# Optimization experiments

Hardware: AMD Instinct MI355X
Metric: run time of the kernel (lower is better)

The kernel has to match this reference:

```python
import jax, jax.numpy as jnp
import numpy as np

B, C_IN, H, W = 2, 256, 48, 48
OC, G, KH, KW, PH, PW = 256, 4, 7, 7, 3, 3


def _patches(y, Hn, Wn):
    # y: (B, C, Hp, Wp) -> (B, C, KH, KW, Hn, Wn); stride=1, dilation=1
    return jnp.stack([
        jnp.stack([y[:, :, i:i + Hn, j:j + Wn] for j in range(KW)], axis=2)
        for i in range(KH)
    ], axis=2)


def setup_inputs() -> dict:
    key = jax.random.key(0)
    k1, k2, k3, k4 = jax.random.split(key, 4)
    fan_out = 3 * OC  # 1x1 conv, kaiming fan_out
    conv_w = jax.random.normal(k2, (3 * OC, C_IN), dtype=jnp.float32) * np.sqrt(2.0 / fan_out).astype(np.float32)
    return {
        "x": jax.random.normal(k1, (B, C_IN, H, W), dtype=jnp.float32),
        "conv_w": conv_w,
        "rpe_h": jax.random.normal(k3, (G, 1, KH, 1, (OC // G) // 2), dtype=jnp.float32),
        "rpe_w": jax.random.normal(k4, (G, 1, 1, KW, (OC // G) // 2), dtype=jnp.float32),
    }


def reference(x, conv_w, rpe_h, rpe_w):
    b, c, h, w = x.shape
    goc = OC // G
    c2 = goc // 2
    K = KH * KW
    center = (K - 1) // 2
    ci, cj = center // KW, center % KW

    # 1x1 conv to 3*OC channels, then zero-pad (equiv. to Conv2d(padding) + bias=False)
    y = jnp.einsum('bchw,oc->bohw', x, conv_w)
    y = jnp.pad(y, ((0, 0), (0, 0), (PH, PH), (PW, PW)))
    Hn = h + 2 * PH - (KH - 1)
    Wn = w + 2 * PW - (KW - 1)
    P = Hn * Wn

    q_full, k_full, v_full = jnp.split(y, 3, axis=1)

    # query: only the center element of each window is used
    query = q_full[:, :, ci:ci + Hn, cj:cj + Wn].reshape(b, G, goc, P)
    query = jnp.transpose(query, (0, 1, 3, 2))  # (B,G,P,goc)

    # key: full windows + relative position embeddings
    kp = _patches(k_full, Hn, Wn).reshape(b, G, goc, KH, KW, P)
    key = jnp.transpose(kp, (0, 1, 5, 3, 4, 2))  # (B,G,P,KH,KW,goc)
    key = jnp.concatenate((key[..., :c2] + rpe_h, key[..., c2:] + rpe_w), axis=1)  # (B,2G,P,KH,KW,c2)
    key = key.reshape(b, G, P, K, goc)  # row-major reshape matches torch

    vp = _patches(v_full, Hn, Wn).reshape(b, G, goc, K, P)
    value = jnp.transpose(vp, (0, 1, 4, 3, 2))  # (B,G,P,K,goc)

    att = jax.nn.softmax(jnp.einsum('bgpc,bgpkc->bgpk', query, key), axis=-1)
    out = jnp.einsum('bgpk,bgpkc->bgpc', att, value)  # (B,G,P,goc)
    out = jnp.transpose(out, (0, 1, 3, 2)).reshape(b, OC, Hn, Wn)
    return out
```

## Files before the change

kernel.cpp:

```cpp
#include <hip/hip_runtime.h>

#define BB   2
#define CIN  256
#define OC3  768
#define NG   4
#define GOC  64
#define C2   32
#define KK   49
#define PP   2304
#define HALF_P 1152

#define RS      56
#define BROWS   54
#define BSTRIDE (BROWS * RS * OC3)
#define IOFF    ((3 * RS + 3) * OC3)

#define Y2_BYTES  (BB * BROWS * RS * OC3 * 4)
#define XT_OFF    Y2_BYTES
#define WT_OFF    (XT_OFF + BB * PP * 512 * 2)

typedef __attribute__((ext_vector_type(8))) short bf16x8;
typedef __attribute__((ext_vector_type(4))) float f32x4;

static __device__ __forceinline__ unsigned short f2bf_rne(float x) {
    unsigned int u = __float_as_uint(x);
    unsigned int r = u + 0x7FFFu + ((u >> 16) & 1u);
    return (unsigned short)(r >> 16);
}
static __device__ __forceinline__ float bf2f(unsigned short h) {
    return __uint_as_float(((unsigned int)h) << 16);
}

#define ROW4  (RS * OC3 / 4)
#define REG1  (6 * ROW4)
#define COLS4 (OC3 / 4)
__global__ __launch_bounds__(256) void zero_guard(float* __restrict__ Y2)
{
    const int idx = blockIdx.x * 256 + threadIdx.x;
    const int b   = blockIdx.y;
    float4* Yb = (float4*)(Y2 + (size_t)b * BSTRIDE);
    const float4 z = make_float4(0.f, 0.f, 0.f, 0.f);
    if (idx < REG1) {
        int r6  = idx / ROW4;
        int rem = idx - r6 * ROW4;
        int r   = (r6 < 3) ? r6 : 48 + r6;
        Yb[r * ROW4 + rem] = z;
    } else {
        int i2  = idx - REG1;
        int r   = 3 + i2 / (8 * COLS4);
        int rem = i2 - (r - 3) * (8 * COLS4);
        int cg  = rem / COLS4;
        int c   = (cg < 3) ? cg : 48 + cg;
        int ch4 = rem - cg * COLS4;
        Yb[(r * RS + c) * COLS4 + ch4] = z;
    }
}

__global__ __launch_bounds__(256) void convert_w(
    const float* __restrict__ W, short* __restrict__ Wt)
{
    int t = blockIdx.x * 256 + threadIdx.x;
    int o = t >> 8, c = t & 255;
    float v = W[t];
    unsigned short hi = f2bf_rne(v);
    unsigned short lo = f2bf_rne(v - bf2f(hi));
    Wt[(size_t)o * 512 + c]       = (short)hi;
    Wt[(size_t)o * 512 + 256 + c] = (short)lo;
}

__global__ __launch_bounds__(256) void convert_x(
    const float* __restrict__ X, short* __restrict__ Xt)
{
    __shared__ float tile[64][65];
    const int t  = threadIdx.x;
    const int p0 = blockIdx.x * 64;
    const int c0 = blockIdx.y * 64;
    const int b  = blockIdx.z;

    const float* Xb = X + (size_t)b * CIN * PP;
    #pragma unroll
    for (int r = 0; r < 16; ++r) {
        int idx = r * 256 + t;
        int c = idx >> 6, p = idx & 63;
        tile[c][p] = Xb[(size_t)(c0 + c) * PP + p0 + p];
    }
    __syncthreads();
    short* Xo = Xt + (size_t)b * PP * 512;
    #pragma unroll
    for (int r = 0; r < 16; ++r) {
        int idx = r * 256 + t;
        int p = idx >> 6, c = idx & 63;
        float v = tile[c][p];
        unsigned short hi = f2bf_rne(v);
        unsigned short lo = f2bf_rne(v - bf2f(hi));
        size_t base = (size_t)(p0 + p) * 512 + c0 + c;
        Xo[base]       = (short)hi;
        Xo[base + 256] = (short)lo;
    }
}

#define LDA 40

__global__ __launch_bounds__(256, 4) void conv_mfma(
    const short* __restrict__ Wt,
    const short* __restrict__ Xt,
    float* __restrict__ Y2)
{
    __shared__ short As[64 * LDA];
    __shared__ short Bs[64 * LDA];

    const int tid = threadIdx.x;
    const int bn  = blockIdx.x;
    const int bm  = blockIdx.y;
    const int b   = blockIdx.z;
    const int om0 = bm * 64, pn0 = bn * 64;

    const int lane = tid & 63, w = tid >> 6;
    const int oq = (w & 1) * 32, pq = (w >> 1) * 32;
    const int ln15 = lane & 15, q = lane >> 4;

    const int  lrow  = (tid & 127) >> 1;
    const int  lsoff = (tid & 1) * 16;
    const bool isA   = tid < 128;
    const short* gA = Wt + (size_t)(om0 + lrow) * 512 + lsoff;
    const short* gB = Xt + (size_t)b * PP * 512 + (size_t)(pn0 + lrow) * 512 + lsoff;
    const short* gsrc = isA ? gA : gB;
    short* ldst = (isA ? As : Bs) + lrow * LDA + lsoff;

    f32x4 acc[2][2] = {};

    for (int k0 = 0; k0 < 768; k0 += 32) {
        const int wk = (k0 < 256) ? k0 : k0 - 256;
        const int xk = (k0 < 512) ? k0 : k0 - 512;
        const int kk = isA ? wk : xk;
        uint4 v0 = *(const uint4*)(gsrc + kk);
        uint4 v1 = *(const uint4*)(gsrc + kk + 8);
        __syncthreads();
        *(uint4*)ldst       = v0;
        *(uint4*)(ldst + 8) = v1;
        __syncthreads();

        bf16x8 af[2], bf[2];
        #pragma unroll
        for (int i = 0; i < 2; ++i) {
            af[i] = *(const bf16x8*)&As[(oq + i * 16 + ln15) * LDA + q * 8];
            bf[i] = *(const bf16x8*)&Bs[(pq + i * 16 + ln15) * LDA + q * 8];
        }
        #pragma unroll
        for (int i = 0; i < 2; ++i)
            #pragma unroll
            for (int j = 0; j < 2; ++j)
                acc[i][j] = __builtin_amdgcn_mfma_f32_16x16x32_bf16(
                    af[i], bf[j], acc[i][j], 0, 0, 0);
    }

    float* Yb = Y2 + (size_t)b * BSTRIDE + IOFF;
    #pragma unroll
    for (int i = 0; i < 2; ++i) {
        #pragma unroll
        for (int j = 0; j < 2; ++j) {
            int o = om0 + oq + i * 16 + q * 4;
            int p = pn0 + pq + j * 16 + ln15;
            int h = p / 48, ww = p - h * 48;
            *(f32x4*)&Yb[(size_t)(h * RS + ww) * OC3 + o] = acc[i][j];
        }
    }
}

struct TagH { static constexpr bool value = true;  };
struct TagW { static constexpr bool value = false; };

__global__ __launch_bounds__(256, 4) void attn_kernel(
    const float* __restrict__ Y2,
    const float* __restrict__ rpe_h,
    const float* __restrict__ rpe_w,
    float* __restrict__ out)
{
    __shared__ float xpose[4][65];

    const int tid  = threadIdx.x;
    const int lane = tid & 63;
    const int w    = tid >> 6;
    const int bx     = blockIdx.x;
    const int wblock = (bx & 7) * 576 + (bx >> 3);
    const int wid    = wblock * 4 + w;
    const int pq   = wid % PP;
    const int g    = (wid / PP) & (NG - 1);
    const int b    = wid / (PP * NG);
    const int ph   = pq / 48;
    const int pw   = pq - ph * 48;

    const float* Yb = Y2 + (size_t)b * BSTRIDE + IOFF;

    const float qv = Yb[(size_t)(ph * RS + pw) * OC3 + g * GOC + lane];

    const int t   = (pq >= HALF_P) ? 1 : 0;
    const int qpr = pq - t * HALF_P;
    const int p0  = 2 * qpr;
    const int ph0 = p0 / 48;
    const int pw0 = p0 - ph0 * 48;
    const int g2  = 2 * g + t;
    const bool use_h = (g2 < NG);
    const int  kch   = use_h ? (CIN + g2 * GOC) : (CIN + (g2 - NG) * GOC + C2);
    const float* rb  = use_h ? (rpe_h + g2 * 7 * C2) : (rpe_w + (g2 - NG) * 7 * C2);

    const int  c  = lane & 31;
    const bool hi = (lane >= 32);

    const float R0 = rb[0 * C2 + c], R1 = rb[1 * C2 + c], R2 = rb[2 * C2 + c],
                R3 = rb[3 * C2 + c], R4 = rb[4 * C2 + c], R5 = rb[5 * C2 + c],
                R6 = rb[6 * C2 + c];

    const float* kb = Yb + (size_t)(ph0 * RS + pw0) * OC3 + kch + c;

    auto rget = [&](int idx) -> float {
        return idx == 0 ? R0 : idx == 1 ? R1 : idx == 2 ? R2 :
               idx == 3 ? R3 : idx == 4 ? R4 : idx == 5 ? R5 : R6;
    };

    auto tree = [&](auto tag) -> float {
        constexpr bool UH = decltype(tag)::value;
        auto chunkprod = [&](int l) -> float {
            int m0 = 2 * l,     h10 = (m0 >= KK), k0 = m0 - KK * h10;
            int m1 = 2 * l + 1, h11 = (m1 >= KK), k1 = m1 - KK * h11;
            int i0 = k0 / 7, j0 = k0 % 7, i1 = k1 / 7, j1 = k1 % 7;
            int d0 = ((i0 - 3) * RS + (h10 + j0 - 3)) * OC3;
            int d1 = ((i1 - 3) * RS + (h11 + j1 - 3)) * OC3;
            float kv = kb[hi ? d1 : d0];
            float ra = UH ? rget(i0) : rget(j0);
            float rc = UH ? rget(i1) : rget(j1);
            kv += hi ? rc : ra;
            return qv * kv;
        };
        float sv[32];
        #pragma unroll
        for (int jj = 0; jj < 32; ++jj) {
            if (2 * jj >= KK) { sv[jj] = 0.f; continue; }
            float pa = chunkprod(2 * jj);
            float pb = (2 * jj + 1 < KK) ? chunkprod(2 * jj + 1) : 0.f;
            float u  = (lane & 1) ? pb : pa;
            float ww = (lane & 1) ? pa : pb;
            sv[jj] = u + __shfl_xor(ww, 1, 64);
        }
        #pragma unroll
        for (int d = 2; d < 64; d <<= 1) {
            #pragma unroll
            for (int i = 0; i < 32; i += d) {
                float a  = sv[i], bb = sv[i + d / 2];
                float u  = (lane & d) ? bb : a;
                float ww = (lane & d) ? a : bb;
                sv[i] = u + __shfl_xor(ww, d, 64);
            }
        }
        return sv[0];
    };

    const float logit = use_h ? tree(TagH{}) : tree(TagW{});

    float mx = logit;
    #pragma unroll
    for (int d = 1; d < 64; d <<= 1)
        mx = fmaxf(mx, __shfl_xor(mx, d, 64));
    float e = (lane < KK) ? __expf(logit - mx) : 0.f;
    float ssum = e;
    #pragma unroll
    for (int d = 1; d < 64; d <<= 1)
        ssum += __shfl_xor(ssum, d, 64);
    const float att = e / ssum;

    float acc = 0.f;
    const float* vb = Yb + (size_t)(ph * RS + pw) * OC3 + 2 * CIN + g * GOC + lane;
    #pragma unroll
    for (int k = 0; k < KK; ++k) {
        int i = k / 7, j = k % 7;
        int doff = ((i - 3) * RS + (j - 3)) * OC3;
        float ak = __uint_as_float(
            __builtin_amdgcn_readlane(__float_as_uint(att), k));
        acc = fmaf(ak, vb[doff], acc);
    }

    xpose[w][lane] = acc;
    __syncthreads();
    const int wid0 = wblock * 4;
    const int pq0  = wid0 % PP;
    const int g0   = (wid0 / PP) & (NG - 1);
    const int b0   = wid0 / (PP * NG);
    const int ch   = tid >> 2;
    const int w2   = tid & 3;
    out[((size_t)b0 * 256 + g0 * GOC + ch) * PP + pq0 + w2] = xpose[w2][ch];
}

extern "C" void kernel_launch(void* const* d_in, const int* in_sizes, int n_in,
                              void* d_out, int out_size, void* d_ws, size_t ws_size,
                              hipStream_t stream)
{
    const float* x  = (const float*)d_in[0];
    const float* w  = (const float*)d_in[1];
    const float* rh = (const float*)d_in[2];
    const float* rw = (const float*)d_in[3];

    float* Y2 = (float*)d_ws;
    short* Xt = (short*)((char*)d_ws + XT_OFF);
    short* Wt = (short*)((char*)d_ws + WT_OFF);

    zero_guard<<<dim3(540, BB), 256, 0, stream>>>(Y2);
    convert_w<<<768, 256, 0, stream>>>(w, Wt);
    convert_x<<<dim3(36, 4, BB), 256, 0, stream>>>(x, Xt);

    conv_mfma<<<dim3(36, 12, BB), 256, 0, stream>>>(Wt, Xt, Y2);

    attn_kernel<<<(BB * NG * PP) / 4, 256, 0, stream>>>(Y2, rh, rw, (float*)d_out);
}
```

Before: 117.4 us.

## Stage attention key/value/query windows in shared memory and merge prep kernels

The attention kernel now cooperatively loads the 7x14 key window, the 7x10 value window and the four queries for its block of adjacent pixels into LDS with float4 loads. Each wave then reads its neighbourhood from shared memory instead of doing strided scalar global loads, so overlapping windows are not fetched again. Separately, the zero-guard, weight-conversion and input-conversion kernels are merged into one launch to cut launch overhead. The cost is more LDS per block, which may lower occupancy, plus an extra block-wide barrier.

New measurement: 123.2 us. 5.0% more time.

```diff
diff --git a/kernel.cpp b/kernel.cpp
--- a/kernel.cpp
+++ b/kernel.cpp
@@ -22,6 +22,9 @@
 typedef __attribute__((ext_vector_type(8))) short bf16x8;
 typedef __attribute__((ext_vector_type(4))) float f32x4;
 
+struct TagH { static constexpr bool value = true;  };
+struct TagW { static constexpr bool value = false; };
+
 static __device__ __forceinline__ unsigned short f2bf_rne(float x) {
     unsigned int u = __float_as_uint(x);
     unsigned int r = u + 0x7FFFu + ((u >> 16) & 1u);
@@ -34,68 +37,65 @@
 #define ROW4  (RS * OC3 / 4)
 #define REG1  (6 * ROW4)
 #define COLS4 (OC3 / 4)
-__global__ __launch_bounds__(256) void zero_guard(float* __restrict__ Y2)
+__global__ __launch_bounds__(256) void prep(
+    const float* __restrict__ X, const float* __restrict__ W,
+    float* __restrict__ Y2, short* __restrict__ Xt, short* __restrict__ Wt)
 {
-    const int idx = blockIdx.x * 256 + threadIdx.x;
-    const int b   = blockIdx.y;
-    float4* Yb = (float4*)(Y2 + (size_t)b * BSTRIDE);
-    const float4 z = make_float4(0.f, 0.f, 0.f, 0.f);
-    if (idx < REG1) {
-        int r6  = idx / ROW4;
-        int rem = idx - r6 * ROW4;
-        int r   = (r6 < 3) ? r6 : 48 + r6;
-        Yb[r * ROW4 + rem] = z;
-    } else {
-        int i2  = idx - REG1;
-        int r   = 3 + i2 / (8 * COLS4);
-        int rem = i2 - (r - 3) * (8 * COLS4);
-        int cg  = rem / COLS4;
-        int c   = (cg < 3) ? cg : 48 + cg;
-        int ch4 = rem - cg * COLS4;
-        Yb[(r * RS + c) * COLS4 + ch4] = z;
-    }
-}
-
-__global__ __launch_bounds__(256) void convert_w(
-    const float* __restrict__ W, short* __restrict__ Wt)
-{
-    int t = blockIdx.x * 256 + threadIdx.x;
-    int o = t >> 8, c = t & 255;
-    float v = W[t];
-    unsigned short hi = f2bf_rne(v);
-    unsigned short lo = f2bf_rne(v - bf2f(hi));
-    Wt[(size_t)o * 512 + c]       = (short)hi;
-    Wt[(size_t)o * 512 + 256 + c] = (short)lo;
-}
-
-__global__ __launch_bounds__(256) void convert_x(
-    const float* __restrict__ X, short* __restrict__ Xt)
-{
-    __shared__ float tile[64][65];
-    const int t  = threadIdx.x;
-    const int p0 = blockIdx.x * 64;
-    const int c0 = blockIdx.y * 64;
-    const int b  = blockIdx.z;
-
-    const float* Xb = X + (size_t)b * CIN * PP;
-    #pragma unroll
-    for (int r = 0; r < 16; ++r) {
-        int idx = r * 256 + t;
-        int c = idx >> 6, p = idx & 63;
-        tile[c][p] = Xb[(size_t)(c0 + c) * PP + p0 + p];
-    }
-    __syncthreads();
-    short* Xo = Xt + (size_t)b * PP * 512;
-    #pragma unroll
-    for (int r = 0; r < 16; ++r) {
-        int idx = r * 256 + t;
-        int p = idx >> 6, c = idx & 63;
-        float v = tile[c][p];
+    const int bxx = blockIdx.x;
+    const int tid = threadIdx.x;
+    if (bxx < 1080) {
+        const int b   = bxx / 540;
+        const int idx = (bxx - b * 540) * 256 + tid;
+        float4* Yb = (float4*)(Y2 + (size_t)b * BSTRIDE);
+        const float4 z = make_float4(0.f, 0.f, 0.f, 0.f);
+        if (idx < REG1) {
+            int r6  = idx / ROW4;
+            int rem = idx - r6 * ROW4;
+            int r   = (r6 < 3) ? r6 : 48 + r6;
+            Yb[r * ROW4 + rem] = z;
+        } else {
+            int i2  = idx - REG1;
+            int r   = 3 + i2 / (8 * COLS4);
+            int rem = i2 - (r - 3) * (8 * COLS4);
+            int cg  = rem / COLS4;
+            int c   = (cg < 3) ? cg : 48 + cg;
+            int ch4 = rem - cg * COLS4;
+            Yb[(r * RS + c) * COLS4 + ch4] = z;
+        }
+    } else if (bxx < 1848) {
+        int t = (bxx - 1080) * 256 + tid;
+        int o = t >> 8, c = t & 255;
+        float v = W[t];
         unsigned short hi = f2bf_rne(v);
         unsigned short lo = f2bf_rne(v - bf2f(hi));
-        size_t base = (size_t)(p0 + p) * 512 + c0 + c;
-        Xo[base]       = (short)hi;
-        Xo[base + 256] = (short)lo;
+        Wt[(size_t)o * 512 + c]       = (short)hi;
+        Wt[(size_t)o * 512 + 256 + c] = (short)lo;
+    } else {
+        __shared__ float tile[64][65];
+        const int cx = bxx - 1848;
+        const int p0 = (cx % 36) * 64;
+        const int c0 = ((cx / 36) & 3) * 64;
+        const int b  = cx / 144;
+        const float* Xb = X + (size_t)b * CIN * PP;
+        #pragma unroll
+        for (int r = 0; r < 16; ++r) {
+            int idx = r * 256 + tid;
+            int c = idx >> 6, p = idx & 63;
+            tile[c][p] = Xb[(size_t)(c0 + c) * PP + p0 + p];
+        }
+        __syncthreads();
+        short* Xo = Xt + (size_t)b * PP * 512;
+        #pragma unroll
+        for (int r = 0; r < 16; ++r) {
+            int idx = r * 256 + tid;
+            int p = idx >> 6, c = idx & 63;
+            float v = tile[c][p];
+            unsigned short hi = f2bf_rne(v);
+            unsigned short lo = f2bf_rne(v - bf2f(hi));
+            size_t base = (size_t)(p0 + p) * 512 + c0 + c;
+            Xo[base]       = (short)hi;
+            Xo[base + 256] = (short)lo;
+        }
     }
 }
 
@@ -167,15 +167,15 @@
     }
 }
 
-struct TagH { static constexpr bool value = true;  };
-struct TagW { static constexpr bool value = false; };
-
 __global__ __launch_bounds__(256, 4) void attn_kernel(
     const float* __restrict__ Y2,
     const float* __restrict__ rpe_h,
     const float* __restrict__ rpe_w,
     float* __restrict__ out)
 {
+    __shared__ float Ks[7 * 14 * 32];
+    __shared__ float Vs[7 * 10 * 64];
+    __shared__ float Qs[4 * 64];
     __shared__ float xpose[4][65];
 
     const int tid  = threadIdx.x;
@@ -183,35 +183,60 @@
     const int w    = tid >> 6;
     const int bx     = blockIdx.x;
     const int wblock = (bx & 7) * 576 + (bx >> 3);
-    const int wid    = wblock * 4 + w;
-    const int pq   = wid % PP;
-    const int g    = (wid / PP) & (NG - 1);
-    const int b    = wid / (PP * NG);
-    const int ph   = pq / 48;
-    const int pw   = pq - ph * 48;
-
-    const float* Yb = Y2 + (size_t)b * BSTRIDE + IOFF;
-
-    const float qv = Yb[(size_t)(ph * RS + pw) * OC3 + g * GOC + lane];
-
-    const int t   = (pq >= HALF_P) ? 1 : 0;
-    const int qpr = pq - t * HALF_P;
-    const int p0  = 2 * qpr;
-    const int ph0 = p0 / 48;
-    const int pw0 = p0 - ph0 * 48;
-    const int g2  = 2 * g + t;
+    const int wid0   = wblock * 4;
+    const int pq0  = wid0 % PP;
+    const int g    = (wid0 / PP) & (NG - 1);
+    const int b    = wid0 / (PP * NG);
+    const int ph   = pq0 / 48;
+    const int pws  = pq0 - ph * 48;
+    const int t    = (pq0 >= HALF_P) ? 1 : 0;
+    const int qp0  = pq0 - t * HALF_P;
+    const int p00  = 2 * qp0;
+    const int ph0  = p00 / 48;
+    const int w0   = p00 - ph0 * 48;
+    const int g2   = 2 * g + t;
     const bool use_h = (g2 < NG);
     const int  kch   = use_h ? (CIN + g2 * GOC) : (CIN + (g2 - NG) * GOC + C2);
-    const float* rb  = use_h ? (rpe_h + g2 * 7 * C2) : (rpe_w + (g2 - NG) * 7 * C2);
+    const int  vch   = 2 * CIN + g * GOC;
+
+    const float* Yb = Y2 + (size_t)b * BSTRIDE + IOFF;
+
+    #pragma unroll
+    for (int it = 0; it < 8; ++it) {
+        int idx = it * 256 + tid;
+        if (idx < 784) {
+            int run = idx >> 3, f4o = idx & 7;
+            int row = run / 14, col = run - row * 14;
+            const float* src = Yb + (long)((ph0 + row - 3) * RS + (w0 + col - 3)) * OC3
+                               + kch + f4o * 4;
+            *(float4*)&Ks[run * 32 + f4o * 4] = *(const float4*)src;
+        } else if (idx < 1904) {
+            int r = idx - 784;
+            int run = r >> 4, f4o = r & 15;
+            int row = run / 10, col = run - row * 10;
+            const float* src = Yb + (long)((ph + row - 3) * RS + (pws + col - 3)) * OC3
+                               + vch + f4o * 4;
+            *(float4*)&Vs[run * 64 + f4o * 4] = *(const float4*)src;
+        } else if (idx < 1968) {
+            int r = idx - 1904;
+            int pi = r >> 4, f4o = r & 15;
+            const float* src = Yb + (long)(ph * RS + pws + pi) * OC3 + g * GOC + f4o * 4;
+            *(float4*)&Qs[pi * 64 + f4o * 4] = *(const float4*)src;
+        }
+    }
 
     const int  c  = lane & 31;
     const bool hi = (lane >= 32);
-
+    const float* rb = use_h ? (rpe_h + g2 * 7 * C2) : (rpe_w + (g2 - NG) * 7 * C2);
     const float R0 = rb[0 * C2 + c], R1 = rb[1 * C2 + c], R2 = rb[2 * C2 + c],
                 R3 = rb[3 * C2 + c], R4 = rb[4 * C2 + c], R5 = rb[5 * C2 + c],
                 R6 = rb[6 * C2 + c];
 
-    const float* kb = Yb + (size_t)(ph0 * RS + pw0) * OC3 + kch + c;
+    __syncthreads();
+
+    const float qv = Qs[w * GOC + lane];
+    const float* kls = Ks + w * 64 + c;
+    const float* vls = Vs + w * 64 + lane;
 
     auto rget = [&](int idx) -> float {
         return idx == 0 ? R0 : idx == 1 ? R1 : idx == 2 ? R2 :
@@ -224,9 +249,9 @@
             int m0 = 2 * l,     h10 = (m0 >= KK), k0 = m0 - KK * h10;
             int m1 = 2 * l + 1, h11 = (m1 >= KK), k1 = m1 - KK * h11;
             int i0 = k0 / 7, j0 = k0 % 7, i1 = k1 / 7, j1 = k1 % 7;
-            int d0 = ((i0 - 3) * RS + (h10 + j0 - 3)) * OC3;
-            int d1 = ((i1 - 3) * RS + (h11 + j1 - 3)) * OC3;
-            float kv = kb[hi ? d1 : d0];
+            int d0 = (i0 * 14 + j0 + h10) * 32;
+            int d1 = (i1 * 14 + j1 + h11) * 32;
+            float kv = kls[hi ? d1 : d0];
             float ra = UH ? rget(i0) : rget(j0);
             float rc = UH ? rget(i1) : rget(j1);
             kv += hi ? rc : ra;
@@ -269,25 +294,19 @@
     const float att = e / ssum;
 
     float acc = 0.f;
-    const float* vb = Yb + (size_t)(ph * RS + pw) * OC3 + 2 * CIN + g * GOC + lane;
     #pragma unroll
     for (int k = 0; k < KK; ++k) {
         int i = k / 7, j = k % 7;
-        int doff = ((i - 3) * RS + (j - 3)) * OC3;
         float ak = __uint_as_float(
             __builtin_amdgcn_readlane(__float_as_uint(att), k));
-        acc = fmaf(ak, vb[doff], acc);
+        acc = fmaf(ak, vls[(i * 10 + j) * 64], acc);
     }
 
     xpose[w][lane] = acc;
     __syncthreads();
-    const int wid0 = wblock * 4;
-    const int pq0  = wid0 % PP;
-    const int g0   = (wid0 / PP) & (NG - 1);
-    const int b0   = wid0 / (PP * NG);
-    const int ch   = tid >> 2;
-    const int w2   = tid & 3;
-    out[((size_t)b0 * 256 + g0 * GOC + ch) * PP + pq0 + w2] = xpose[w2][ch];
+    const int ch = tid >> 2;
+    const int w2 = tid & 3;
+    out[((size_t)b * 256 + g * GOC + ch) * PP + pq0 + w2] = xpose[w2][ch];
 }
 
 extern "C" void kernel_launch(void* const* d_in, const int* in_sizes, int n_in,
@@ -303,11 +322,7 @@
     short* Xt = (short*)((char*)d_ws + XT_OFF);
     short* Wt = (short*)((char*)d_ws + WT_OFF);
 
-    zero_guard<<<dim3(540, BB), 256, 0, stream>>>(Y2);
-    convert_w<<<768, 256, 0, stream>>>(w, Wt);
-    convert_x<<<dim3(36, 4, BB), 256, 0, stream>>>(x, Xt);
-
+    prep<<<2136, 256, 0, stream>>>(x, w, Y2, Xt, Wt);
     conv_mfma<<<dim3(36, 12, BB), 256, 0, stream>>>(Wt, Xt, Y2);
-
     attn_kernel<<<(BB * NG * PP) / 4, 256, 0, stream>>>(Y2, rh, rw, (float*)d_out);
 }
```
